# Performance work log

Hardware: AMD Instinct MI355X
Metric: run time of the kernel (lower is better)

The kernel has to match this reference:

```python
import jax, jax.numpy as jnp
import numpy as np

B, E, H, V, KV = 64, 256, 512, 50257, 2048


def setup_inputs() -> dict:
    key = jax.random.key(0)
    ks = jax.random.split(key, 16)
    s_e = 1.0 / np.sqrt(E)
    s_h = 1.0 / np.sqrt(H)
    s_eh = 1.0 / np.sqrt(E + H)
    return {
        "input": jax.random.randint(ks[0], (B,), 0, V),
        "h0": jax.random.normal(ks[1], (B, H), jnp.float32),
        "c0": jax.random.normal(ks[2], (B, H), jnp.float32),
        "k": jax.random.normal(ks[3], (KV, E), jnp.float32),
        "context_vector": jax.random.normal(ks[4], (B, H), jnp.float32),
        # embedding table
        "embedding": jax.random.normal(ks[5], (V, E), jnp.float32) * 0.02,
        # LSTMCell params (PyTorch layout: gates ordered i,f,g,o)
        "W_ih": jax.random.uniform(ks[6], (4 * H, E), jnp.float32, -s_h, s_h),
        "b_ih": jax.random.uniform(ks[7], (4 * H,), jnp.float32, -s_h, s_h),
        "W_hh": jax.random.uniform(ks[8], (4 * H, H), jnp.float32, -s_h, s_h),
        "b_hh": jax.random.uniform(ks[9], (4 * H,), jnp.float32, -s_h, s_h),
        # attn_key MLP: Linear(E+H,E) -> tanh -> Linear(E,E) -> tanh -> Linear(E,1)
        "W1": jax.random.uniform(ks[10], (E, E + H), jnp.float32, -s_eh, s_eh),
        "b1": jnp.zeros((E,), jnp.float32),
        "W2": jax.random.uniform(ks[11], (E, E), jnp.float32, -s_e, s_e),
        "b2": jnp.zeros((E,), jnp.float32),
        "W3": jax.random.uniform(ks[12], (1, E), jnp.float32, -s_e, s_e),
        "b3": jnp.zeros((1,), jnp.float32),
        # output projection Linear(H, V)
        "W_out": jax.random.uniform(ks[13], (V, H), jnp.float32, -s_h, s_h),
        "b_out": jax.random.uniform(ks[14], (V,), jnp.float32, -s_h, s_h),
    }


def reference(input, h0, c0, k, context_vector, embedding, W_ih, b_ih, W_hh, b_hh,
              W1, b1, W2, b2, W3, b3, W_out, b_out):
    # embedding lookup (dropout in eval mode = identity)
    x = embedding[input]  # (B, E)
    # LSTMCell
    gates = x @ W_ih.T + b_ih + h0 @ W_hh.T + b_hh  # (B, 4H)
    i, f, g, o = jnp.split(gates, 4, axis=-1)
    i = jax.nn.sigmoid(i)
    f = jax.nn.sigmoid(f)
    g = jnp.tanh(g)
    o = jax.nn.sigmoid(o)
    c_t = f * c0 + i * g
    h_t = o * jnp.tanh(c_t)  # (B, H)
    # key attention: broadcast h_t over kv keys, keys over batch (torch.cat-repeat in original)
    h_b = jnp.broadcast_to(h_t[:, None, :], (B, KV, H))
    k_b = jnp.broadcast_to(k[None, :, :], (B, KV, E))
    feat = jnp.concatenate([h_b, k_b], axis=-1)  # (B, KV, H+E)
    u = jnp.tanh(feat @ W1.T + b1)
    u = jnp.tanh(u @ W2.T + b2)
    scores = (u @ W3.T + b3)[..., 0]  # (B, KV)
    # vocab logits; original pads V-KV zeros in front then adds -> scores hit last KV slots
    o_t = h_t @ W_out.T + b_out  # (B, V)
    o_t = o_t.at[:, V - KV:].add(scores)
    y_t = jax.nn.log_softmax(o_t, axis=-1)
    return (y_t, h_t, c_t)
```

## Files before the change

kernel.cpp:

```cpp
#include <hip/hip_runtime.h>
#include <math.h>

namespace {

constexpr int B = 64, E = 256, H = 512, V = 50257, KV = 2048;
constexpr int NOUT = (V + 63) / 64;
constexpr int VP = NOUT * 64;
constexpr int PSTRIDE = 800;
constexpr int NPACK = (VP / 32);

typedef __bf16 bf16x8 __attribute__((ext_vector_type(8)));
typedef float f32x4 __attribute__((ext_vector_type(4)));

__device__ __forceinline__ float fast_tanh(float x) {
  float e = __expf(2.f * x);
  return 1.f - 2.f / (e + 1.f);
}
__device__ __forceinline__ float sigmoidf(float x) {
  return 1.f / (1.f + __expf(-x));
}
__device__ __forceinline__ f32x4 mfma16(bf16x8 a, bf16x8 b, f32x4 c) {
  return __builtin_amdgcn_mfma_f32_16x16x32_bf16(a, b, c, 0, 0, 0);
}

__global__ __launch_bounds__(256) void k_cell(const int* __restrict__ inp,
    const float* __restrict__ h0, const float* __restrict__ c0,
    const float* __restrict__ emb,
    const float* __restrict__ W_ih, const float* __restrict__ b_ih,
    const float* __restrict__ W_hh, const float* __restrict__ b_hh,
    float* __restrict__ h_t, float* __restrict__ c_t, __bf16* __restrict__ hp) {
  __shared__ float g4[4][64];
  int tid = threadIdx.x;
  int hh = blockIdx.x;
  int jq = tid >> 6, b = tid & 63;
  int j = jq * 512 + hh;
  int row = inp[b];
  const float* xr = emb + (long)row * E;
  const float* wi = W_ih + (long)j * E;
  const float* hr = h0 + (long)b * H;
  const float* wh = W_hh + (long)j * H;
  float acc = b_ih[j] + b_hh[j];
#pragma unroll 8
  for (int q = 0; q < E / 4; ++q) {
    float4 x4 = ((const float4*)xr)[q];
    float4 w4 = ((const float4*)wi)[q];
    acc += x4.x * w4.x + x4.y * w4.y + x4.z * w4.z + x4.w * w4.w;
  }
#pragma unroll 8
  for (int q = 0; q < H / 4; ++q) {
    float4 h4 = ((const float4*)hr)[q];
    float4 w4 = ((const float4*)wh)[q];
    acc += h4.x * w4.x + h4.y * w4.y + h4.z * w4.z + h4.w * w4.w;
  }
  g4[jq][b] = acc;
  __syncthreads();
  if (tid < 64) {
    int bb = tid;
    float cc = sigmoidf(g4[1][bb]) * c0[bb * H + hh] +
               sigmoidf(g4[0][bb]) * fast_tanh(g4[2][bb]);
    float hv = sigmoidf(g4[3][bb]) * fast_tanh(cc);
    h_t[bb * H + hh] = hv;
    c_t[bb * H + hh] = cc;
    hp[((hh >> 3) * 64 + bb) * 8 + (hh & 7)] = (__bf16)hv;
  }
}

__global__ __launch_bounds__(256) void k_prep(const float* __restrict__ h_t,
    const float* __restrict__ W1, const float* __restrict__ b1,
    const float* __restrict__ k, const float* __restrict__ W2,
    float* __restrict__ Ah, float* __restrict__ Kp, __bf16* __restrict__ W2p) {
  __shared__ float ks_[64][257];
  int bid = blockIdx.x;
  int t = threadIdx.x;
  if (bid < 64) {
    int b = t & 63;
    int e = bid * 4 + (t >> 6);
    e = __builtin_amdgcn_readfirstlane(e);
    const float* hr = h_t + b * H;
    const float* wr = W1 + (long)e * (E + H);
    float acc = b1[e];
#pragma unroll 8
    for (int q = 0; q < H / 4; ++q) {
      float4 h4 = ((const float4*)hr)[q];
      float4 w4 = ((const float4*)wr)[q];
      acc += h4.x * w4.x + h4.y * w4.y + h4.z * w4.z + h4.w * w4.w;
    }
    Ah[b * E + e] = acc;
  } else if (bid < 192) {
    int t2 = bid - 64;
    int kv0 = (t2 & 31) * 64;
    int e0 = (t2 >> 5) * 64;
    for (int i = 0; i < 16; ++i) {
      int idx = i * 256 + t;
      int rr = idx >> 6, cc = (idx & 63) * 4;
      float4 v = *(const float4*)(k + (kv0 + rr) * E + cc);
      ks_[rr][cc] = v.x; ks_[rr][cc + 1] = v.y; ks_[rr][cc + 2] = v.z; ks_[rr][cc + 3] = v.w;
    }
    __syncthreads();
    int r0 = (t >> 4);
    int c0 = (t & 15) * 4;
    float acc[4][4] = {};
    const float* w0 = W1 + (long)(e0 + c0) * (E + H) + H;
    for (int kk = 0; kk < 256; kk += 4) {
      float4 w[4];
#pragma unroll
      for (int c = 0; c < 4; ++c) w[c] = *(const float4*)(w0 + (long)c * (E + H) + kk);
#pragma unroll
      for (int q = 0; q < 4; ++q) {
#pragma unroll
        for (int r = 0; r < 4; ++r) {
          float kvv = ks_[r0 + 16 * r][kk + q];
#pragma unroll
          for (int c = 0; c < 4; ++c) acc[r][c] += kvv * ((const float*)&w[c])[q];
        }
      }
    }
    for (int r = 0; r < 4; ++r)
      for (int c = 0; c < 4; ++c)
        Kp[(kv0 + r0 + 16 * r) * E + e0 + c0 + c] = acc[r][c];
  } else {
    int idx = (bid - 192) * 256 + t;
    int kk = idx >> 8, n = idx & 255;
    W2p[((kk >> 3) * 256 + n) * 8 + (kk & 7)] = (__bf16)W2[n * 256 + kk];
  }
}

__global__ __launch_bounds__(512, 4) void k_attnpw(const float* __restrict__ Ah,
    const float* __restrict__ Kp, const __bf16* __restrict__ W2p,
    const float* __restrict__ b2, const float* __restrict__ W3, const float* __restrict__ b3,
    const float* __restrict__ W_out,
    float* __restrict__ scoresT, __bf16* __restrict__ Wp) {
  __shared__ __align__(16) unsigned char lds_[32768];
  __shared__ float red2[64][8];
  int tid = threadIdx.x;
  int blk = blockIdx.x;
  if (blk >= 2048) {
    int col0 = (blk - 2048) * 32;
#pragma unroll
    for (int i = 0; i < 4; ++i) {
      int u = i * 512 + tid;
      int row = u >> 6, k8 = u & 63;
      int rr = col0 + row; if (rr > V - 1) rr = V - 1;
      const float* p = W_out + (long)rr * H + k8 * 8;
      float4 w0 = *(const float4*)p;
      float4 w1 = *(const float4*)(p + 4);
      bf16x8 v;
      v[0] = (__bf16)w0.x; v[1] = (__bf16)w0.y; v[2] = (__bf16)w0.z; v[3] = (__bf16)w0.w;
      v[4] = (__bf16)w1.x; v[5] = (__bf16)w1.y; v[6] = (__bf16)w1.z; v[7] = (__bf16)w1.w;
      int byte = (row * 1024 + k8 * 16) ^ ((row & 7) << 4);
      *(bf16x8*)(lds_ + byte) = v;
    }
    __syncthreads();
#pragma unroll
    for (int i = 0; i < 4; ++i) {
      int u = i * 512 + tid;
      int k8 = u >> 5, colt = u & 31;
      int byte = (colt * 1024 + k8 * 16) ^ ((colt & 7) << 4);
      bf16x8 v = *(const bf16x8*)(lds_ + byte);
      *(bf16x8*)(Wp + ((long)k8 * VP + col0 + colt) * 8) = v;
    }
    return;
  }
  int b = blk >> 5;
  int kv0 = (blk & 31) * 64;
#pragma unroll
  for (int i = 0; i < 4; ++i) {
    int idx = i * 512 + tid;
    int row = idx >> 5;
    int k0 = (idx & 31) * 8;
    const float* ap = Ah + b * E + k0;
    const float* kp = Kp + (kv0 + row) * E + k0;
    float4 a0 = *(const float4*)ap;
    float4 a1 = *(const float4*)(ap + 4);
    float4 p0 = *(const float4*)kp;
    float4 p1 = *(const float4*)(kp + 4);
    bf16x8 u;
    u[0] = (__bf16)fast_tanh(a0.x + p0.x);
    u[1] = (__bf16)fast_tanh(a0.y + p0.y);
    u[2] = (__bf16)fast_tanh(a0.z + p0.z);
    u[3] = (__bf16)fast_tanh(a0.w + p0.w);
    u[4] = (__bf16)fast_tanh(a1.x + p1.x);
    u[5] = (__bf16)fast_tanh(a1.y + p1.y);
    u[6] = (__bf16)fast_tanh(a1.z + p1.z);
    u[7] = (__bf16)fast_tanh(a1.w + p1.w);
    int byte = (row * 512 + k0 * 2) ^ ((row & 7) << 4);
    *(bf16x8*)(lds_ + byte) = u;
  }
  __syncthreads();
  int w = tid >> 6;
  int l = tid & 63;
  int lr = l & 15, lg = l >> 4;
  float b2v[2], w3v[2];
#pragma unroll
  for (int nf = 0; nf < 2; ++nf) {
    int col = w * 32 + nf * 16 + lr;
    b2v[nf] = b2[col];
    w3v[nf] = W3[col];
  }
  f32x4 acc[4][2] = {};
  bf16x8 bf_n[2];
#pragma unroll
  for (int nf = 0; nf < 2; ++nf)
    bf_n[nf] = *(const bf16x8*)(W2p + ((0 * 4 + lg) * 256 + w * 32 + nf * 16 + lr) * 8);
#pragma unroll
  for (int ks = 0; ks < 8; ++ks) {
    bf16x8 a[4], bf_c[2];
    bf_c[0] = bf_n[0]; bf_c[1] = bf_n[1];
    if (ks < 7) {
#pragma unroll
      for (int nf = 0; nf < 2; ++nf)
        bf_n[nf] = *(const bf16x8*)(W2p + (((ks + 1) * 4 + lg) * 256 + w * 32 + nf * 16 + lr) * 8);
    }
#pragma unroll
    for (int mf = 0; mf < 4; ++mf) {
      int row = mf * 16 + lr;
      int byte = (row * 512 + (ks * 32 + lg * 8) * 2) ^ ((row & 7) << 4);
      a[mf] = *(const bf16x8*)(lds_ + byte);
    }
#pragma unroll
    for (int mf = 0; mf < 4; ++mf)
#pragma unroll
      for (int nf = 0; nf < 2; ++nf)
        acc[mf][nf] = mfma16(a[mf], bf_c[nf], acc[mf][nf]);
  }
  float p[4][4];
#pragma unroll
  for (int mf = 0; mf < 4; ++mf)
#pragma unroll
    for (int r = 0; r < 4; ++r) p[mf][r] = 0.f;
#pragma unroll
  for (int mf = 0; mf < 4; ++mf)
#pragma unroll
    for (int nf = 0; nf < 2; ++nf)
#pragma unroll
      for (int r = 0; r < 4; ++r) {
        float u2 = fast_tanh(acc[mf][nf][r] + b2v[nf]);
        p[mf][r] += u2 * w3v[nf];
      }
#pragma unroll
  for (int off = 1; off < 16; off <<= 1)
#pragma unroll
    for (int mf = 0; mf < 4; ++mf)
#pragma unroll
      for (int r = 0; r < 4; ++r) p[mf][r] += __shfl_xor(p[mf][r], off);
  if (lr == 0) {
#pragma unroll
    for (int mf = 0; mf < 4; ++mf)
#pragma unroll
      for (int r = 0; r < 4; ++r) red2[mf * 16 + lg * 4 + r][w] = p[mf][r];
  }
  __syncthreads();
  if (tid < 64) {
    float s = b3[0];
#pragma unroll
    for (int ww = 0; ww < 8; ++ww) s += red2[tid][ww];
    scoresT[(kv0 + tid) * 64 + b] = s;
  }
}

__global__ __launch_bounds__(256, 4) void k_out(const __bf16* __restrict__ hp,
    const __bf16* __restrict__ Wp, const float* __restrict__ b_out,
    const float* __restrict__ scoresT, float* __restrict__ o,
    float* __restrict__ pm, float* __restrict__ ps) {
  __shared__ float vbuf[64][65];
  __shared__ float rm[64][4], rs[64][4];
  int tid = threadIdx.x;
  int l = tid & 63, wn = tid >> 6;
  int lr = l & 15, lg = l >> 4;
  int col0 = blockIdx.x * 64;
  int col = col0 + wn * 16 + lr;
  f32x4 acc[4] = {};
  bf16x8 a_n[4], b_n;
#pragma unroll
  for (int mf = 0; mf < 4; ++mf)
    a_n[mf] = *(const bf16x8*)(hp + ((0 * 4 + lg) * 64 + mf * 16 + lr) * 8);
  b_n = *(const bf16x8*)(Wp + ((long)(0 * 4 + lg) * VP + col) * 8);
#pragma unroll
  for (int ks = 0; ks < 16; ++ks) {
    bf16x8 a_c[4]; bf16x8 b_c = b_n;
#pragma unroll
    for (int mf = 0; mf < 4; ++mf) a_c[mf] = a_n[mf];
    if (ks < 15) {
      int ksg = ks + 1;
#pragma unroll
      for (int mf = 0; mf < 4; ++mf)
        a_n[mf] = *(const bf16x8*)(hp + ((ksg * 4 + lg) * 64 + mf * 16 + lr) * 8);
      b_n = *(const bf16x8*)(Wp + ((long)(ksg * 4 + lg) * VP + col) * 8);
    }
#pragma unroll
    for (int mf = 0; mf < 4; ++mf) acc[mf] = mfma16(a_c[mf], b_c, acc[mf]);
  }
  bool valid = col < V;
  float bo = valid ? b_out[col] : 0.f;
  bool has = valid && col >= (V - KV);
  int scix = col - (V - KV);
#pragma unroll
  for (int mf = 0; mf < 4; ++mf)
#pragma unroll
    for (int r = 0; r < 4; ++r) {
      int m = mf * 16 + lg * 4 + r;
      float v = acc[mf][r] + bo;
      if (has) v += scoresT[scix * 64 + m];
      if (!valid) v = -1e30f;
      vbuf[m][wn * 16 + lr] = v;
    }
  __syncthreads();
  int nvalid = V - col0; if (nvalid > 64) nvalid = 64;
#pragma unroll
  for (int i = 0; i < 16; ++i) {
    int idx = i * 256 + tid;
    int m = idx >> 6, c = idx & 63;
    if (c < nvalid) o[(long)m * V + col0 + c] = vbuf[m][c];
  }
  int row = tid & 63, g = tid >> 6;
  float mm = -1e30f;
#pragma unroll
  for (int c = 0; c < 16; ++c) mm = fmaxf(mm, vbuf[row][g * 16 + c]);
  float ssum = 0.f;
#pragma unroll
  for (int c = 0; c < 16; ++c) ssum += __expf(vbuf[row][g * 16 + c] - mm);
  rm[row][g] = mm; rs[row][g] = ssum;
  __syncthreads();
  if (tid < 64) {
    float M = fmaxf(fmaxf(rm[tid][0], rm[tid][1]), fmaxf(rm[tid][2], rm[tid][3]));
    float S = 0.f;
#pragma unroll
    for (int g2 = 0; g2 < 4; ++g2) S += rs[tid][g2] * __expf(rm[tid][g2] - M);
    pm[tid * PSTRIDE + blockIdx.x] = M;
    ps[tid * PSTRIDE + blockIdx.x] = S;
  }
}

__global__ __launch_bounds__(256) void k_subz(const float* __restrict__ pm,
    const float* __restrict__ ps, float* __restrict__ y) {
  __shared__ float sm[4], ss[4];
  __shared__ float zz;
  int r = blockIdx.y;
  int tid = threadIdx.x;
  float m = -1e30f, s = 0.f;
  for (int p = tid; p < NOUT; p += 256) {
    float om = pm[r * PSTRIDE + p];
    float os = ps[r * PSTRIDE + p];
    float M = fmaxf(m, om);
    s = s * __expf(m - M) + os * __expf(om - M);
    m = M;
  }
#pragma unroll
  for (int off = 1; off < 64; off <<= 1) {
    float om = __shfl_xor(m, off);
    float os = __shfl_xor(s, off);
    float M = fmaxf(m, om);
    s = s * __expf(m - M) + os * __expf(om - M);
    m = M;
  }
  int w = tid >> 6;
  if ((tid & 63) == 0) { sm[w] = m; ss[w] = s; }
  __syncthreads();
  if (tid == 0) {
    m = sm[0]; s = ss[0];
    for (int i = 1; i < 4; ++i) {
      float M = fmaxf(m, sm[i]);
      s = s * __expf(m - M) + ss[i] * __expf(sm[i] - M);
      m = M;
    }
    zz = m + __logf(s);
  }
  __syncthreads();
  float z = zz;
  float* rowp = y + (long)r * V;
#pragma unroll
  for (int i = 0; i < 4; ++i) {
    int c = blockIdx.x * 4096 + i * 1024 + tid * 4;
    if (c + 3 < V) {
      float4 v = *(float4*)(rowp + c);
      v.x -= z; v.y -= z; v.z -= z; v.w -= z;
      *(float4*)(rowp + c) = v;
    } else {
      for (int c2 = c; c2 < V; ++c2) rowp[c2] -= z;
    }
  }
}

}

extern "C" void kernel_launch(void* const* d_in, const int* in_sizes, int n_in,
                              void* d_out, int out_size, void* d_ws, size_t ws_size,
                              hipStream_t stream) {
  const int* inp = (const int*)d_in[0];
  const float* h0 = (const float*)d_in[1];
  const float* c0 = (const float*)d_in[2];
  const float* kk = (const float*)d_in[3];
  const float* emb = (const float*)d_in[5];
  const float* W_ih = (const float*)d_in[6];
  const float* b_ih = (const float*)d_in[7];
  const float* W_hh = (const float*)d_in[8];
  const float* b_hh = (const float*)d_in[9];
  const float* W1 = (const float*)d_in[10];
  const float* b1 = (const float*)d_in[11];
  const float* W2 = (const float*)d_in[12];
  const float* b2 = (const float*)d_in[13];
  const float* W3 = (const float*)d_in[14];
  const float* b3 = (const float*)d_in[15];
  const float* W_out = (const float*)d_in[16];
  const float* b_out = (const float*)d_in[17];

  float* y = (float*)d_out;
  float* h_t = y + (size_t)B * V;
  float* c_t = h_t + (size_t)B * H;

  char* ws = (char*)d_ws;
  float* Ah = (float*)ws;                    ws += (size_t)B * E * 4;
  float* Kp = (float*)ws;                    ws += (size_t)KV * E * 4;
  float* scoresT = (float*)ws;               ws += (size_t)B * KV * 4;
  float* pm = (float*)ws;                    ws += (size_t)B * PSTRIDE * 4;
  float* ps = (float*)ws;                    ws += (size_t)B * PSTRIDE * 4;
  __bf16* W2p = (__bf16*)ws;                 ws += (size_t)E * E * 2;
  __bf16* hp = (__bf16*)ws;                  ws += (size_t)B * H * 2;
  ws = (char*)(((size_t)ws + 255) & ~(size_t)255);
  __bf16* Wp = (__bf16*)ws;                  ws += (size_t)VP * H * 2;

  hipLaunchKernelGGL(k_cell, dim3(H), dim3(256), 0, stream,
                     inp, h0, c0, emb, W_ih, b_ih, W_hh, b_hh, h_t, c_t, hp);
  hipLaunchKernelGGL(k_prep, dim3(448), dim3(256), 0, stream,
                     h_t, W1, b1, kk, W2, Ah, Kp, W2p);
  hipLaunchKernelGGL(k_attnpw, dim3(2048 + NPACK), dim3(512), 0, stream,
                     Ah, Kp, W2p, b2, W3, b3, W_out, scoresT, Wp);
  hipLaunchKernelGGL(k_out, dim3(NOUT), dim3(256), 0, stream,
                     hp, Wp, b_out, scoresT, y, pm, ps);
  hipLaunchKernelGGL(k_subz, dim3(13, B), dim3(256), 0, stream, pm, ps, y);
}
```

Baseline: 177.3 us.

## Restructure attention MLP kernel to per-wave row tiles held in registers

The attention score kernel now runs 256-thread blocks in which each wave owns 16 KV rows. The wave builds the tanh(Ah+Kp) A-fragments directly in registers, so the LDS staging, the cross-wave reduction buffer and two block barriers are gone. Each wave loops over all 16 column tiles of W2 and reads W2p fragments straight from global or cache, which means more global reads per wave in exchange for no LDS traffic. The W_out packing blocks are moved to the front of the grid so that long memory-bound work is scheduled first, and each packing block now handles twice as many iterations with half the threads.

```diff
diff --git a/kernel.cpp b/kernel.cpp
--- a/kernel.cpp
+++ b/kernel.cpp
@@ -7,7 +7,7 @@
 constexpr int NOUT = (V + 63) / 64;
 constexpr int VP = NOUT * 64;
 constexpr int PSTRIDE = 800;
-constexpr int NPACK = (VP / 32);
+constexpr int NPACK = VP / 32;
 
 typedef __bf16 bf16x8 __attribute__((ext_vector_type(8)));
 typedef float f32x4 __attribute__((ext_vector_type(4)));
@@ -125,20 +125,19 @@
   }
 }
 
-__global__ __launch_bounds__(512, 4) void k_attnpw(const float* __restrict__ Ah,
+__global__ __launch_bounds__(256, 5) void k_attnpw(const float* __restrict__ Ah,
     const float* __restrict__ Kp, const __bf16* __restrict__ W2p,
     const float* __restrict__ b2, const float* __restrict__ W3, const float* __restrict__ b3,
     const float* __restrict__ W_out,
     float* __restrict__ scoresT, __bf16* __restrict__ Wp) {
   __shared__ __align__(16) unsigned char lds_[32768];
-  __shared__ float red2[64][8];
   int tid = threadIdx.x;
   int blk = blockIdx.x;
-  if (blk >= 2048) {
-    int col0 = (blk - 2048) * 32;
-#pragma unroll
-    for (int i = 0; i < 4; ++i) {
-      int u = i * 512 + tid;
+  if (blk < NPACK) {
+    int col0 = blk * 32;
+#pragma unroll
+    for (int i = 0; i < 8; ++i) {
+      int u = i * 256 + tid;
       int row = u >> 6, k8 = u & 63;
       int rr = col0 + row; if (rr > V - 1) rr = V - 1;
       const float* p = W_out + (long)rr * H + k8 * 8;
@@ -152,8 +151,8 @@
     }
     __syncthreads();
 #pragma unroll
-    for (int i = 0; i < 4; ++i) {
-      int u = i * 512 + tid;
+    for (int i = 0; i < 8; ++i) {
+      int u = i * 256 + tid;
       int k8 = u >> 5, colt = u & 31;
       int byte = (colt * 1024 + k8 * 16) ^ ((colt & 7) << 4);
       bf16x8 v = *(const bf16x8*)(lds_ + byte);
@@ -161,19 +160,20 @@
     }
     return;
   }
-  int b = blk >> 5;
-  int kv0 = (blk & 31) * 64;
-#pragma unroll
-  for (int i = 0; i < 4; ++i) {
-    int idx = i * 512 + tid;
-    int row = idx >> 5;
-    int k0 = (idx & 31) * 8;
-    const float* ap = Ah + b * E + k0;
-    const float* kp = Kp + (kv0 + row) * E + k0;
-    float4 a0 = *(const float4*)ap;
-    float4 a1 = *(const float4*)(ap + 4);
-    float4 p0 = *(const float4*)kp;
-    float4 p1 = *(const float4*)(kp + 4);
+  int ablk = blk - NPACK;
+  int b = ablk >> 5;
+  int kvw = (ablk & 31) * 64 + (tid >> 6) * 16;
+  int l = tid & 63, lr = l & 15, lg = l >> 4;
+  bf16x8 au[8];
+  const float* ah = Ah + b * E;
+  const float* kp = Kp + (long)(kvw + lr) * E;
+#pragma unroll
+  for (int ks = 0; ks < 8; ++ks) {
+    int e0 = ks * 32 + lg * 8;
+    float4 a0 = *(const float4*)(ah + e0);
+    float4 a1 = *(const float4*)(ah + e0 + 4);
+    float4 p0 = *(const float4*)(kp + e0);
+    float4 p1 = *(const float4*)(kp + e0 + 4);
     bf16x8 u;
     u[0] = (__bf16)fast_tanh(a0.x + p0.x);
     u[1] = (__bf16)fast_tanh(a0.y + p0.y);
@@ -183,78 +183,32 @@
     u[5] = (__bf16)fast_tanh(a1.y + p1.y);
     u[6] = (__bf16)fast_tanh(a1.z + p1.z);
     u[7] = (__bf16)fast_tanh(a1.w + p1.w);
-    int byte = (row * 512 + k0 * 2) ^ ((row & 7) << 4);
-    *(bf16x8*)(lds_ + byte) = u;
-  }
-  __syncthreads();
-  int w = tid >> 6;
-  int l = tid & 63;
-  int lr = l & 15, lg = l >> 4;
-  float b2v[2], w3v[2];
-#pragma unroll
-  for (int nf = 0; nf < 2; ++nf) {
-    int col = w * 32 + nf * 16 + lr;
-    b2v[nf] = b2[col];
-    w3v[nf] = W3[col];
-  }
-  f32x4 acc[4][2] = {};
-  bf16x8 bf_n[2];
-#pragma unroll
-  for (int nf = 0; nf < 2; ++nf)
-    bf_n[nf] = *(const bf16x8*)(W2p + ((0 * 4 + lg) * 256 + w * 32 + nf * 16 + lr) * 8);
-#pragma unroll
-  for (int ks = 0; ks < 8; ++ks) {
-    bf16x8 a[4], bf_c[2];
-    bf_c[0] = bf_n[0]; bf_c[1] = bf_n[1];
-    if (ks < 7) {
-#pragma unroll
-      for (int nf = 0; nf < 2; ++nf)
-        bf_n[nf] = *(const bf16x8*)(W2p + (((ks + 1) * 4 + lg) * 256 + w * 32 + nf * 16 + lr) * 8);
-    }
-#pragma unroll
-    for (int mf = 0; mf < 4; ++mf) {
-      int row = mf * 16 + lr;
-      int byte = (row * 512 + (ks * 32 + lg * 8) * 2) ^ ((row & 7) << 4);
-      a[mf] = *(const bf16x8*)(lds_ + byte);
-    }
-#pragma unroll
-    for (int mf = 0; mf < 4; ++mf)
-#pragma unroll
-      for (int nf = 0; nf < 2; ++nf)
-        acc[mf][nf] = mfma16(a[mf], bf_c[nf], acc[mf][nf]);
-  }
-  float p[4][4];
-#pragma unroll
-  for (int mf = 0; mf < 4; ++mf)
-#pragma unroll
-    for (int r = 0; r < 4; ++r) p[mf][r] = 0.f;
-#pragma unroll
-  for (int mf = 0; mf < 4; ++mf)
-#pragma unroll
-    for (int nf = 0; nf < 2; ++nf)
-#pragma unroll
-      for (int r = 0; r < 4; ++r) {
-        float u2 = fast_tanh(acc[mf][nf][r] + b2v[nf]);
-        p[mf][r] += u2 * w3v[nf];
-      }
+    au[ks] = u;
+  }
+  float p[4] = {0.f, 0.f, 0.f, 0.f};
+#pragma unroll 2
+  for (int nt = 0; nt < 16; ++nt) {
+    int col = nt * 16 + lr;
+    float b2v = b2[col];
+    float w3v = W3[col];
+    f32x4 acc = {0.f, 0.f, 0.f, 0.f};
+#pragma unroll
+    for (int ks = 0; ks < 8; ++ks) {
+      bf16x8 bf = *(const bf16x8*)(W2p + ((ks * 4 + lg) * 256 + col) * 8);
+      acc = mfma16(au[ks], bf, acc);
+    }
+#pragma unroll
+    for (int r = 0; r < 4; ++r) p[r] += fast_tanh(acc[r] + b2v) * w3v;
+  }
 #pragma unroll
   for (int off = 1; off < 16; off <<= 1)
 #pragma unroll
-    for (int mf = 0; mf < 4; ++mf)
-#pragma unroll
-      for (int r = 0; r < 4; ++r) p[mf][r] += __shfl_xor(p[mf][r], off);
+    for (int r = 0; r < 4; ++r) p[r] += __shfl_xor(p[r], off);
   if (lr == 0) {
-#pragma unroll
-    for (int mf = 0; mf < 4; ++mf)
-#pragma unroll
-      for (int r = 0; r < 4; ++r) red2[mf * 16 + lg * 4 + r][w] = p[mf][r];
-  }
-  __syncthreads();
-  if (tid < 64) {
-    float s = b3[0];
-#pragma unroll
-    for (int ww = 0; ww < 8; ++ww) s += red2[tid][ww];
-    scoresT[(kv0 + tid) * 64 + b] = s;
+    float bb3 = b3[0];
+#pragma unroll
+    for (int r = 0; r < 4; ++r)
+      scoresT[(kvw + lg * 4 + r) * 64 + b] = p[r] + bb3;
   }
 }
 
@@ -423,7 +377,7 @@
                      inp, h0, c0, emb, W_ih, b_ih, W_hh, b_hh, h_t, c_t, hp);
   hipLaunchKernelGGL(k_prep, dim3(448), dim3(256), 0, stream,
                      h_t, W1, b1, kk, W2, Ah, Kp, W2p);
-  hipLaunchKernelGGL(k_attnpw, dim3(2048 + NPACK), dim3(512), 0, stream,
+  hipLaunchKernelGGL(k_attnpw, dim3(NPACK + 2048), dim3(256), 0, stream,
                      Ah, Kp, W2p, b2, W3, b3, W_out, scoresT, Wp);
   hipLaunchKernelGGL(k_out, dim3(NOUT), dim3(256), 0, stream,
                      hp, Wp, b_out, scoresT, y, pm, ps);
```

Result: slower. 209.8 us (+18.3%).

## Move W_out packing into prep kernel and stage W tile via global_load_lds in k_out

Applied to the files above, without the earlier changes.

The W_out fp32-to-bf16 packing moves out of the attention kernel and into the prep kernel, as 64-column blocks that use 64KB of LDS. The attention kernel becomes pure attention scoring. k_out now preloads its whole 64-column by 512-K bf16 weight tile into LDS with async global_load_lds before the MFMA loop, instead of prefetching from global per k-step. The larger LDS footprints lower occupancy in both kernels, and the packing now competes with the Kp projection instead of the attention MLP.

```diff
diff --git a/kernel.cpp b/kernel.cpp
--- a/kernel.cpp
+++ b/kernel.cpp
@@ -7,7 +7,6 @@
 constexpr int NOUT = (V + 63) / 64;
 constexpr int VP = NOUT * 64;
 constexpr int PSTRIDE = 800;
-constexpr int NPACK = (VP / 32);
 
 typedef __bf16 bf16x8 __attribute__((ext_vector_type(8)));
 typedef float f32x4 __attribute__((ext_vector_type(4)));
@@ -21,6 +20,11 @@
 }
 __device__ __forceinline__ f32x4 mfma16(bf16x8 a, bf16x8 b, f32x4 c) {
   return __builtin_amdgcn_mfma_f32_16x16x32_bf16(a, b, c, 0, 0, 0);
+}
+__device__ __forceinline__ void gload_lds16(const void* g, void* l) {
+  __builtin_amdgcn_global_load_lds(
+      (const __attribute__((address_space(1))) unsigned int*)g,
+      (__attribute__((address_space(3))) unsigned int*)l, 16, 0, 0);
 }
 
 __global__ __launch_bounds__(256) void k_cell(const int* __restrict__ inp,
@@ -65,11 +69,13 @@
   }
 }
 
-__global__ __launch_bounds__(256) void k_prep(const float* __restrict__ h_t,
+__global__ __launch_bounds__(256) void k_preppw(const float* __restrict__ h_t,
     const float* __restrict__ W1, const float* __restrict__ b1,
     const float* __restrict__ k, const float* __restrict__ W2,
-    float* __restrict__ Ah, float* __restrict__ Kp, __bf16* __restrict__ W2p) {
-  __shared__ float ks_[64][257];
+    const float* __restrict__ W_out,
+    float* __restrict__ Ah, float* __restrict__ Kp, __bf16* __restrict__ W2p,
+    __bf16* __restrict__ Wp) {
+  __shared__ __align__(16) unsigned char SM[65792];
   int bid = blockIdx.x;
   int t = threadIdx.x;
   if (bid < 64) {
@@ -87,6 +93,7 @@
     }
     Ah[b * E + e] = acc;
   } else if (bid < 192) {
+    float (*ks_)[257] = (float(*)[257])SM;
     int t2 = bid - 64;
     int kv0 = (t2 & 31) * 64;
     int e0 = (t2 >> 5) * 64;
@@ -118,27 +125,16 @@
     for (int r = 0; r < 4; ++r)
       for (int c = 0; c < 4; ++c)
         Kp[(kv0 + r0 + 16 * r) * E + e0 + c0 + c] = acc[r][c];
+  } else if (bid < 448) {
+    int idx = (bid - 192) * 256 + t;
+    int kk2 = idx >> 8, n = idx & 255;
+    W2p[((kk2 >> 3) * 256 + n) * 8 + (kk2 & 7)] = (__bf16)W2[n * 256 + kk2];
   } else {
-    int idx = (bid - 192) * 256 + t;
-    int kk = idx >> 8, n = idx & 255;
-    W2p[((kk >> 3) * 256 + n) * 8 + (kk & 7)] = (__bf16)W2[n * 256 + kk];
-  }
-}
-
-__global__ __launch_bounds__(512, 4) void k_attnpw(const float* __restrict__ Ah,
-    const float* __restrict__ Kp, const __bf16* __restrict__ W2p,
-    const float* __restrict__ b2, const float* __restrict__ W3, const float* __restrict__ b3,
-    const float* __restrict__ W_out,
-    float* __restrict__ scoresT, __bf16* __restrict__ Wp) {
-  __shared__ __align__(16) unsigned char lds_[32768];
-  __shared__ float red2[64][8];
-  int tid = threadIdx.x;
-  int blk = blockIdx.x;
-  if (blk >= 2048) {
-    int col0 = (blk - 2048) * 32;
-#pragma unroll
-    for (int i = 0; i < 4; ++i) {
-      int u = i * 512 + tid;
+    unsigned char* lds_ = SM;
+    int col0 = (bid - 448) * 64;
+#pragma unroll
+    for (int i = 0; i < 16; ++i) {
+      int u = i * 256 + t;
       int row = u >> 6, k8 = u & 63;
       int rr = col0 + row; if (rr > V - 1) rr = V - 1;
       const float* p = W_out + (long)rr * H + k8 * 8;
@@ -152,15 +148,24 @@
     }
     __syncthreads();
 #pragma unroll
-    for (int i = 0; i < 4; ++i) {
-      int u = i * 512 + tid;
-      int k8 = u >> 5, colt = u & 31;
+    for (int i = 0; i < 16; ++i) {
+      int u = i * 256 + t;
+      int k8 = u >> 6, colt = u & 63;
       int byte = (colt * 1024 + k8 * 16) ^ ((colt & 7) << 4);
       bf16x8 v = *(const bf16x8*)(lds_ + byte);
       *(bf16x8*)(Wp + ((long)k8 * VP + col0 + colt) * 8) = v;
     }
-    return;
-  }
+  }
+}
+
+__global__ __launch_bounds__(512, 4) void k_attn(const float* __restrict__ Ah,
+    const float* __restrict__ Kp, const __bf16* __restrict__ W2p,
+    const float* __restrict__ b2, const float* __restrict__ W3, const float* __restrict__ b3,
+    float* __restrict__ scoresT) {
+  __shared__ __align__(16) unsigned char lds_[32768];
+  __shared__ float red2[64][8];
+  int tid = threadIdx.x;
+  int blk = blockIdx.x;
   int b = blk >> 5;
   int kv0 = (blk & 31) * 64;
 #pragma unroll
@@ -258,38 +263,46 @@
   }
 }
 
-__global__ __launch_bounds__(256, 4) void k_out(const __bf16* __restrict__ hp,
+__global__ __launch_bounds__(256) void k_out(const __bf16* __restrict__ hp,
     const __bf16* __restrict__ Wp, const float* __restrict__ b_out,
     const float* __restrict__ scoresT, float* __restrict__ o,
     float* __restrict__ pm, float* __restrict__ ps) {
-  __shared__ float vbuf[64][65];
+  __shared__ __align__(16) unsigned char lds_[65536];
   __shared__ float rm[64][4], rs[64][4];
   int tid = threadIdx.x;
   int l = tid & 63, wn = tid >> 6;
   int lr = l & 15, lg = l >> 4;
   int col0 = blockIdx.x * 64;
-  int col = col0 + wn * 16 + lr;
+  {
+    const __bf16* wsrc = Wp + ((long)(wn * 16) * VP + col0 + l) * 8;
+    unsigned char* ldst = lds_ + wn * 16 * 1024;
+#pragma unroll
+    for (int i = 0; i < 16; ++i)
+      gload_lds16(wsrc + (long)i * VP * 8, ldst + i * 1024);
+  }
   f32x4 acc[4] = {};
-  bf16x8 a_n[4], b_n;
+  bf16x8 a_n[4];
 #pragma unroll
   for (int mf = 0; mf < 4; ++mf)
     a_n[mf] = *(const bf16x8*)(hp + ((0 * 4 + lg) * 64 + mf * 16 + lr) * 8);
-  b_n = *(const bf16x8*)(Wp + ((long)(0 * 4 + lg) * VP + col) * 8);
+  __syncthreads();
 #pragma unroll
   for (int ks = 0; ks < 16; ++ks) {
-    bf16x8 a_c[4]; bf16x8 b_c = b_n;
+    bf16x8 a_c[4];
 #pragma unroll
     for (int mf = 0; mf < 4; ++mf) a_c[mf] = a_n[mf];
     if (ks < 15) {
-      int ksg = ks + 1;
 #pragma unroll
       for (int mf = 0; mf < 4; ++mf)
-        a_n[mf] = *(const bf16x8*)(hp + ((ksg * 4 + lg) * 64 + mf * 16 + lr) * 8);
-      b_n = *(const bf16x8*)(Wp + ((long)(ksg * 4 + lg) * VP + col) * 8);
-    }
-#pragma unroll
-    for (int mf = 0; mf < 4; ++mf) acc[mf] = mfma16(a_c[mf], b_c, acc[mf]);
-  }
+        a_n[mf] = *(const bf16x8*)(hp + (((ks + 1) * 4 + lg) * 64 + mf * 16 + lr) * 8);
+    }
+    bf16x8 bv = *(const bf16x8*)(lds_ + (ks * 4 + lg) * 1024 + (wn * 16 + lr) * 16);
+#pragma unroll
+    for (int mf = 0; mf < 4; ++mf) acc[mf] = mfma16(a_c[mf], bv, acc[mf]);
+  }
+  __syncthreads();
+  float (*vbuf)[65] = (float(*)[65])lds_;
+  int col = col0 + wn * 16 + lr;
   bool valid = col < V;
   float bo = valid ? b_out[col] : 0.f;
   bool has = valid && col >= (V - KV);
@@ -421,10 +434,10 @@
 
   hipLaunchKernelGGL(k_cell, dim3(H), dim3(256), 0, stream,
                      inp, h0, c0, emb, W_ih, b_ih, W_hh, b_hh, h_t, c_t, hp);
-  hipLaunchKernelGGL(k_prep, dim3(448), dim3(256), 0, stream,
-                     h_t, W1, b1, kk, W2, Ah, Kp, W2p);
-  hipLaunchKernelGGL(k_attnpw, dim3(2048 + NPACK), dim3(512), 0, stream,
-                     Ah, Kp, W2p, b2, W3, b3, W_out, scoresT, Wp);
+  hipLaunchKernelGGL(k_preppw, dim3(448 + NOUT), dim3(256), 0, stream,
+                     h_t, W1, b1, kk, W2, W_out, Ah, Kp, W2p, Wp);
+  hipLaunchKernelGGL(k_attn, dim3(B * KV / 64), dim3(512), 0, stream,
+                     Ah, Kp, W2p, b2, W3, b3, scoresT);
   hipLaunchKernelGGL(k_out, dim3(NOUT), dim3(256), 0, stream,
                      hp, Wp, b_out, scoresT, y, pm, ps);
   hipLaunchKernelGGL(k_subz, dim3(13, B), dim3(256), 0, stream, pm, ps, y);
```

Measured after the change: 177.4 us. Within noise of the previous version (+0.0%).
